# Kernel tuning notes

Hardware: AMD Instinct MI355X
Metric: run time of the kernel (lower is better)

Reference implementation:

```python
import jax, jax.numpy as jnp
import numpy as np

B, S, DQ, DK, D, H, L = 32768, 8, 64, 512, 64, 4, 4
DH = D * H  # concat head dim = 256
EPS = 1e-5
SCALE = 1.0 / float(np.sqrt(D))  # torch scales by sqrt(key.size(-1)) == sqrt(n_dim)


def _ln(x, g, b):
    m = x.mean(-1, keepdims=True)
    v = ((x - m) ** 2).mean(-1, keepdims=True)
    return (x - m) / jnp.sqrt(v + EPS) * g + b


def _mha(q, k, v, Wq, bq, Wk, bk, Wv, bv, Wo, bo):
    nb = q.shape[0]
    def tr(x, W, b):
        # [nb, s, in] -> [nb, H, s, D] (head-major split matches torch .view)
        return (x @ W + b).reshape(nb, -1, H, D).transpose(0, 2, 1, 3)
    Q, K, V = tr(q, Wq, bq), tr(k, Wk, bk), tr(v, Wv, bv)
    prob = jax.nn.softmax(jnp.einsum('bhqd,bhkd->bhqk', Q, K) * SCALE, axis=-1)
    out = jnp.einsum('bhqk,bhkd->bhqd', prob, V).transpose(0, 2, 1, 3).reshape(nb, -1, DH)
    return out @ Wo + bo, prob


def setup_inputs() -> dict:
    ki = iter(jax.random.split(jax.random.key(0), 64))
    def w(shape, fan_in):
        return jax.random.normal(next(ki), shape, jnp.float32) / np.float32(np.sqrt(fan_in))
    return {
        'query': jax.random.normal(next(ki), (B, 1, DQ), jnp.float32),
        'latent': jax.random.normal(next(ki), (B, S, DK), jnp.float32),
        'W1': w((DK, D), DK), 'b1': jnp.zeros((D,), jnp.float32),
        'Wq': w((L, D, DH), D), 'bq': jnp.zeros((L, DH), jnp.float32),
        'Wk': w((L, D, DH), D), 'bk': jnp.zeros((L, DH), jnp.float32),
        'Wv': w((L, D, DH), D), 'bv': jnp.zeros((L, DH), jnp.float32),
        'Wo': w((L, DH, D), DH), 'bo': jnp.zeros((L, D), jnp.float32),
        'fW1': w((L, D, D), D), 'fb1': jnp.zeros((L, D), jnp.float32),
        'fW2': w((L, D, D), D), 'fb2': jnp.zeros((L, D), jnp.float32),
        'g1': jnp.ones((L, D), jnp.float32), 'be1': jnp.zeros((L, D), jnp.float32),
        'g2': jnp.ones((L, D), jnp.float32), 'be2': jnp.zeros((L, D), jnp.float32),
        'cWq': w((DQ, DH), DQ), 'cbq': jnp.zeros((DH,), jnp.float32),
        'cWk': w((D, DH), D), 'cbk': jnp.zeros((DH,), jnp.float32),
        'cWv': w((D, DH), D), 'cbv': jnp.zeros((DH,), jnp.float32),
        'cWo': w((DH, D), DH), 'cbo': jnp.zeros((D,), jnp.float32),
        'Wc': w((D, 3), D), 'bc': jnp.zeros((3,), jnp.float32),
        'Ws': w((D, 1), D), 'bs': jnp.zeros((1,), jnp.float32),
    }


def reference(query, latent, W1, b1, Wq, bq, Wk, bk, Wv, bv, Wo, bo,
              fW1, fb1, fW2, fb2, g1, be1, g2, be2,
              cWq, cbq, cWk, cbk, cWv, cbv, cWo, cbo, Wc, bc, Ws, bs):
    out = jax.nn.relu(latent @ W1 + b1)  # [B, S, D]
    probs = []
    for i in range(L):
        a, p = _mha(out, out, out, Wq[i], bq[i], Wk[i], bk[i], Wv[i], bv[i], Wo[i], bo[i])
        out = _ln(a + out, g1[i], be1[i])
        ff = jax.nn.relu(out @ fW1[i] + fb1[i]) @ fW2[i] + fb2[i]  # dropout is eval-mode identity
        out = _ln(ff + out, g2[i], be2[i])
        probs.append(p)
    attn = jnp.stack(probs, axis=1)  # [B, L, H, S, S]
    sigma = jnp.max(out, axis=1) @ Ws + bs  # [B, 1]
    ca, _ = _mha(query, out, out, cWq, cbq, cWk, cbk, cWv, cbv, cWo, cbo)
    color = jax.nn.relu(ca) @ Wc + bc  # [B, 1, 3]
    return color, sigma, out, attn
```

## Files before the change

### kernel.cpp

```cpp
#include <hip/hip_runtime.h>

typedef unsigned short u16;
#define DEV __device__ __forceinline__

constexpr int B_  = 32768;
constexpr int S_  = 8;
constexpr int DK_ = 512;
constexpr int D_  = 64;
constexpr int H_  = 4;
constexpr int DH_ = 256;
constexpr int L_  = 4;
constexpr float SCALE_ = 0.125f;
constexpr float EPS_   = 1e-5f;

DEV float wsum(float x){
    #pragma unroll
    for (int m=1; m<64; m<<=1) x += __shfl_xor(x, m, 64);
    return x;
}

struct P {
    const float *query,*latent,*W1,*b1,*Wq,*bq,*Wk,*bk,*Wv,*bv,*Wo,*bo,
                *fW1,*fb1,*fW2,*fb2,*g1,*be1,*g2,*be2,
                *cWq,*cbq,*cWk,*cbk,*cWv,*cbv,*cWo,*cbo,*Wc,*bc,*Ws,*bs;
    float *o_color,*o_sigma,*o_out,*o_attn;
};

constexpr int WLDS = 512 + 2080 + 2080 + 256;

__global__ __launch_bounds__(128) void rt_fused(P p){
    __shared__ float sh[2*WLDS];
    const int wave = threadIdx.x >> 6;
    const int lane = threadIdx.x & 63;
    const int b    = blockIdx.x*2 + wave;
    float* so   = sh + wave*WLDS;
    float* bufA = so   + 512;
    float* bufK = bufA + 2080;
    float* bufP = bufK + 2080;

    float o[8];
    {
        float* lat = so;
        const float4* latv = (const float4*)(p.latent + (size_t)b*(S_*DK_));
        float4* lat4 = (float4*)lat;
        #pragma unroll
        for (int k=0;k<16;++k) lat4[k*64+lane] = latv[k*64+lane];
        __syncthreads();
        float acc[8];
        #pragma unroll
        for (int s=0;s<8;++s) acc[s] = p.b1[lane];
        #pragma unroll 4
        for (int c=0;c<512;++c){
            float w = p.W1[c*64 + lane];
            #pragma unroll
            for (int s=0;s<8;++s) acc[s] = fmaf(lat[s*512+c], w, acc[s]);
        }
        #pragma unroll
        for (int s=0;s<8;++s) o[s] = fmaxf(acc[s], 0.f);
        __syncthreads();
    }

    float v[4][8];
    for (int i=0;i<L_;++i){
        const float* Wq_i = p.Wq + (size_t)i*D_*DH_;
        const float* Wk_i = p.Wk + (size_t)i*D_*DH_;
        const float* Wv_i = p.Wv + (size_t)i*D_*DH_;
        const float* bq_i = p.bq + i*DH_;
        const float* bk_i = p.bk + i*DH_;
        const float* bv_i = p.bv + i*DH_;
        const float* Wo_i = p.Wo + (size_t)i*DH_*D_;
        const float* bo_i = p.bo + i*D_;
        const float* fW1_i= p.fW1+ i*D_*D_;
        const float* fb1_i= p.fb1+ i*D_;
        const float* fW2_i= p.fW2+ i*D_*D_;
        const float* fb2_i= p.fb2+ i*D_;
        const float* g1_i = p.g1 + i*D_;
        const float* be1_i= p.be1+ i*D_;
        const float* g2_i = p.g2 + i*D_;
        const float* be2_i= p.be2+ i*D_;

        #pragma unroll
        for (int s=0;s<8;++s) so[s*64+lane] = o[s];
        __syncthreads();

        for (int h=0;h<4;++h){
            float aq[8], ak[8], av[8];
            float bqv = bq_i[h*64+lane], bkv = bk_i[h*64+lane], bvv = bv_i[h*64+lane];
            #pragma unroll
            for (int s=0;s<8;++s){ aq[s]=bqv; ak[s]=bkv; av[s]=bvv; }
            #pragma unroll 4
            for (int c=0;c<64;++c){
                int wi = c*256 + h*64 + lane;
                float wq=Wq_i[wi], wk=Wk_i[wi], wv=Wv_i[wi];
                #pragma unroll
                for (int s=0;s<8;++s){
                    float ov = so[s*64+c];
                    aq[s]=fmaf(ov,wq,aq[s]); ak[s]=fmaf(ov,wk,ak[s]); av[s]=fmaf(ov,wv,av[s]);
                }
            }
            #pragma unroll
            for (int s=0;s<8;++s){
                bufA[(h*8+s)*65+lane]=aq[s];
                bufK[(h*8+s)*65+lane]=ak[s];
                v[h][s]=av[s];
            }
        }
        __syncthreads();

        {
            const int q = lane>>3, kk = lane&7;
            #pragma unroll
            for (int h=0;h<4;++h){
                float sc=0.f;
                #pragma unroll 8
                for (int d=0;d<64;++d) sc = fmaf(bufA[(h*8+q)*65+d], bufK[(h*8+kk)*65+d], sc);
                sc *= SCALE_;
                float mx = sc;
                mx=fmaxf(mx,__shfl_xor(mx,1,64));
                mx=fmaxf(mx,__shfl_xor(mx,2,64));
                mx=fmaxf(mx,__shfl_xor(mx,4,64));
                float e=__expf(sc-mx);
                float sm=e;
                sm+=__shfl_xor(sm,1,64); sm+=__shfl_xor(sm,2,64); sm+=__shfl_xor(sm,4,64);
                float pr=e/sm;
                p.o_attn[(size_t)b*1024 + i*256 + h*64 + lane] = pr;
                bufP[h*64+lane]=pr;
            }
        }
        __syncthreads();

        #pragma unroll
        for (int h=0;h<4;++h){
            #pragma unroll
            for (int s=0;s<8;++s){
                float acc=0.f;
                #pragma unroll
                for (int k2=0;k2<8;++k2) acc = fmaf(bufP[h*64+s*8+k2], v[h][k2], acc);
                bufA[s*256 + h*64 + lane] = acc;
            }
        }
        __syncthreads();

        {
            float acc[8];
            float bv2 = bo_i[lane];
            #pragma unroll
            for (int s=0;s<8;++s) acc[s]=bv2;
            #pragma unroll 4
            for (int p2=0;p2<256;++p2){
                float w = Wo_i[p2*64 + lane];
                #pragma unroll
                for (int s=0;s<8;++s) acc[s]=fmaf(bufA[s*256+p2], w, acc[s]);
            }
            float g=g1_i[lane], be=be1_i[lane];
            #pragma unroll
            for (int s=0;s<8;++s){
                float x = acc[s] + o[s];
                float m = wsum(x)*(1.f/64.f);
                float xm = x-m;
                float var = wsum(xm*xm)*(1.f/64.f);
                o[s] = xm*rsqrtf(var+EPS_)*g + be;
            }
        }
        __syncthreads();

        #pragma unroll
        for (int s=0;s<8;++s) so[s*64+lane]=o[s];
        __syncthreads();
        {
            float acc[8];
            float bv2=fb1_i[lane];
            #pragma unroll
            for (int s=0;s<8;++s) acc[s]=bv2;
            #pragma unroll 4
            for (int c=0;c<64;++c){
                float w=fW1_i[c*64+lane];
                #pragma unroll
                for (int s=0;s<8;++s) acc[s]=fmaf(so[s*64+c], w, acc[s]);
            }
            #pragma unroll
            for (int s=0;s<8;++s) bufK[s*64+lane]=fmaxf(acc[s],0.f);
        }
        __syncthreads();
        {
            float acc[8];
            float bv2=fb2_i[lane];
            #pragma unroll
            for (int s=0;s<8;++s) acc[s]=bv2;
            #pragma unroll 4
            for (int c=0;c<64;++c){
                float w=fW2_i[c*64+lane];
                #pragma unroll
                for (int s=0;s<8;++s) acc[s]=fmaf(bufK[s*64+c], w, acc[s]);
            }
            float g=g2_i[lane], be=be2_i[lane];
            #pragma unroll
            for (int s=0;s<8;++s){
                float x = acc[s]+o[s];
                float m=wsum(x)*(1.f/64.f);
                float xm=x-m;
                float var=wsum(xm*xm)*(1.f/64.f);
                o[s]=xm*rsqrtf(var+EPS_)*g+be;
            }
        }
        __syncthreads();
    }

    #pragma unroll
    for (int s=0;s<8;++s) p.o_out[(size_t)b*512 + s*64 + lane] = o[s];

    {
        float mx=o[0];
        #pragma unroll
        for (int s=1;s<8;++s) mx=fmaxf(mx,o[s]);
        float part = mx*p.Ws[lane];
        float sg = wsum(part) + p.bs[0];
        if (lane==0) p.o_sigma[b]=sg;
    }

    #pragma unroll
    for (int s=0;s<8;++s) so[s*64+lane]=o[s];
    bufP[lane]=p.query[(size_t)b*64 + lane];
    __syncthreads();

    float vc[4][8];
    for (int h=0;h<4;++h){
        {
            float aq=p.cbq[h*64+lane];
            #pragma unroll 4
            for (int c=0;c<64;++c) aq=fmaf(bufP[c], p.cWq[c*256 + h*64+lane], aq);
            bufA[h*65+lane]=aq;
        }
        float ak[8], av[8];
        float bkv=p.cbk[h*64+lane], bvv=p.cbv[h*64+lane];
        #pragma unroll
        for (int s=0;s<8;++s){ ak[s]=bkv; av[s]=bvv; }
        #pragma unroll 4
        for (int c=0;c<64;++c){
            int wi=c*256+h*64+lane;
            float wk=p.cWk[wi], wv=p.cWv[wi];
            #pragma unroll
            for (int s=0;s<8;++s){
                float ov=so[s*64+c];
                ak[s]=fmaf(ov,wk,ak[s]); av[s]=fmaf(ov,wv,av[s]);
            }
        }
        #pragma unroll
        for (int s=0;s<8;++s){ bufK[(h*8+s)*65+lane]=ak[s]; vc[h][s]=av[s]; }
    }
    __syncthreads();

    {
        const int hh=(lane>>3)&3, k2=lane&7;
        float sc=0.f;
        #pragma unroll 8
        for (int d=0;d<64;++d) sc=fmaf(bufA[hh*65+d], bufK[(hh*8+k2)*65+d], sc);
        sc*=SCALE_;
        float mx=sc;
        mx=fmaxf(mx,__shfl_xor(mx,1,64));
        mx=fmaxf(mx,__shfl_xor(mx,2,64));
        mx=fmaxf(mx,__shfl_xor(mx,4,64));
        float e=__expf(sc-mx);
        float sm=e;
        sm+=__shfl_xor(sm,1,64); sm+=__shfl_xor(sm,2,64); sm+=__shfl_xor(sm,4,64);
        float pr=e/sm;
        if (lane<32) bufP[lane]=pr;
    }
    __syncthreads();

    #pragma unroll
    for (int h=0;h<4;++h){
        float acc=0.f;
        #pragma unroll
        for (int k2=0;k2<8;++k2) acc=fmaf(bufP[h*8+k2], vc[h][k2], acc);
        bufA[h*64+lane]=acc;
    }
    __syncthreads();

    {
        float acc=p.cbo[lane];
        #pragma unroll 4
        for (int p2=0;p2<256;++p2) acc=fmaf(bufA[p2], p.cWo[p2*64+lane], acc);
        float r=fmaxf(acc,0.f);
        float c0=wsum(r*p.Wc[lane*3+0]);
        float c1=wsum(r*p.Wc[lane*3+1]);
        float c2=wsum(r*p.Wc[lane*3+2]);
        if (lane==0){
            p.o_color[(size_t)b*3+0]=c0+p.bc[0];
            p.o_color[(size_t)b*3+1]=c1+p.bc[1];
            p.o_color[(size_t)b*3+2]=c2+p.bc[2];
        }
    }
}

extern "C" void kernel_launch(void* const* d_in, const int* in_sizes, int n_in,
                              void* d_out, int out_size, void* d_ws, size_t ws_size,
                              hipStream_t stream){
    const float* const* ins = (const float* const*)d_in;
    P p;
    p.query=ins[0];  p.latent=ins[1]; p.W1=ins[2];   p.b1=ins[3];
    p.Wq=ins[4];     p.bq=ins[5];     p.Wk=ins[6];   p.bk=ins[7];
    p.Wv=ins[8];     p.bv=ins[9];     p.Wo=ins[10];  p.bo=ins[11];
    p.fW1=ins[12];   p.fb1=ins[13];   p.fW2=ins[14]; p.fb2=ins[15];
    p.g1=ins[16];    p.be1=ins[17];   p.g2=ins[18];  p.be2=ins[19];
    p.cWq=ins[20];   p.cbq=ins[21];   p.cWk=ins[22]; p.cbk=ins[23];
    p.cWv=ins[24];   p.cbv=ins[25];   p.cWo=ins[26]; p.cbo=ins[27];
    p.Wc=ins[28];    p.bc=ins[29];    p.Ws=ins[30];  p.bs=ins[31];
    float* out=(float*)d_out;
    p.o_color = out;
    p.o_sigma = out + (size_t)B_*3;
    p.o_out   = out + (size_t)B_*4;
    p.o_attn  = out + (size_t)B_*4 + (size_t)B_*512;
    hipLaunchKernelGGL(rt_fused, dim3(B_/2), dim3(128), 0, stream, p);
}
```

Before: 6.628 ms.

## Replace LDS staging with readlane broadcasts and fuse attention into Wo projection

Rewrites the whole fused kernel so activations stay in registers and are broadcast with readlane instead of being staged through shared memory with block barriers. The latent input is streamed in 64-column chunks with prefetch, Q/K/V are computed two heads at a time, attention output is folded straight into the Wo accumulation, and the cross-attention is recomputed per head entirely in registers. Blocks now hold 4 waves with a small per-wave LDS footprint to raise occupancy. The cost is many scalar readlane operations and higher register pressure, which could limit occupancy.

Result: faster. 6.184 ms (-6.7%).

```diff
diff --git a/kernel.cpp b/kernel.cpp
--- a/kernel.cpp
+++ b/kernel.cpp
@@ -1,17 +1,14 @@
 #include <hip/hip_runtime.h>
 
-typedef unsigned short u16;
 #define DEV __device__ __forceinline__
 
-constexpr int B_  = 32768;
-constexpr int S_  = 8;
-constexpr int DK_ = 512;
-constexpr int D_  = 64;
-constexpr int H_  = 4;
-constexpr int DH_ = 256;
-constexpr int L_  = 4;
+constexpr int B_ = 32768;
 constexpr float SCALE_ = 0.125f;
 constexpr float EPS_   = 1e-5f;
+
+DEV float rl(float x, int l){
+    return __int_as_float(__builtin_amdgcn_readlane(__float_as_int(x), l));
+}
 
 DEV float wsum(float x){
     #pragma unroll
@@ -26,269 +23,270 @@
     float *o_color,*o_sigma,*o_out,*o_attn;
 };
 
-constexpr int WLDS = 512 + 2080 + 2080 + 256;
-
-__global__ __launch_bounds__(128) void rt_fused(P p){
-    __shared__ float sh[2*WLDS];
+constexpr int WROW = 68;
+constexpr int WLDS = 2*8*WROW;
+
+__global__ __launch_bounds__(256,4) void rt_fused(P p){
+    __shared__ __align__(16) float sh[4*WLDS];
     const int wave = threadIdx.x >> 6;
     const int lane = threadIdx.x & 63;
-    const int b    = blockIdx.x*2 + wave;
-    float* so   = sh + wave*WLDS;
-    float* bufA = so   + 512;
-    float* bufK = bufA + 2080;
-    float* bufP = bufK + 2080;
+    const int b    = (blockIdx.x<<2) + wave;
+    float* lq = sh + wave*WLDS;
+    float* lk = lq + 8*WROW;
 
     float o[8];
     {
-        float* lat = so;
-        const float4* latv = (const float4*)(p.latent + (size_t)b*(S_*DK_));
-        float4* lat4 = (float4*)lat;
-        #pragma unroll
-        for (int k=0;k<16;++k) lat4[k*64+lane] = latv[k*64+lane];
-        __syncthreads();
+        const float* latb = p.latent + ((size_t)b<<12) + lane;
+        float lat[8];
+        #pragma unroll
+        for (int s=0;s<8;++s) lat[s] = latb[s*512];
         float acc[8];
-        #pragma unroll
-        for (int s=0;s<8;++s) acc[s] = p.b1[lane];
-        #pragma unroll 4
-        for (int c=0;c<512;++c){
-            float w = p.W1[c*64 + lane];
-            #pragma unroll
-            for (int s=0;s<8;++s) acc[s] = fmaf(lat[s*512+c], w, acc[s]);
+        float bb = p.b1[lane];
+        #pragma unroll
+        for (int s=0;s<8;++s) acc[s] = bb;
+        #pragma unroll 1
+        for (int cb=0; cb<8; ++cb){
+            float nlat[8];
+            if (cb < 7){
+                #pragma unroll
+                for (int s=0;s<8;++s) nlat[s] = latb[s*512 + (cb+1)*64];
+            }
+            const float* w1 = p.W1 + cb*64*64 + lane;
+            #pragma unroll 2
+            for (int c=0;c<64;++c){
+                float w = w1[c*64];
+                #pragma unroll
+                for (int s=0;s<8;++s) acc[s] = fmaf(rl(lat[s],c), w, acc[s]);
+            }
+            #pragma unroll
+            for (int s=0;s<8;++s) lat[s] = nlat[s];
         }
         #pragma unroll
         for (int s=0;s<8;++s) o[s] = fmaxf(acc[s], 0.f);
-        __syncthreads();
-    }
-
-    float v[4][8];
-    for (int i=0;i<L_;++i){
-        const float* Wq_i = p.Wq + (size_t)i*D_*DH_;
-        const float* Wk_i = p.Wk + (size_t)i*D_*DH_;
-        const float* Wv_i = p.Wv + (size_t)i*D_*DH_;
-        const float* bq_i = p.bq + i*DH_;
-        const float* bk_i = p.bk + i*DH_;
-        const float* bv_i = p.bv + i*DH_;
-        const float* Wo_i = p.Wo + (size_t)i*DH_*D_;
-        const float* bo_i = p.bo + i*D_;
-        const float* fW1_i= p.fW1+ i*D_*D_;
-        const float* fb1_i= p.fb1+ i*D_;
-        const float* fW2_i= p.fW2+ i*D_*D_;
-        const float* fb2_i= p.fb2+ i*D_;
-        const float* g1_i = p.g1 + i*D_;
-        const float* be1_i= p.be1+ i*D_;
-        const float* g2_i = p.g2 + i*D_;
-        const float* be2_i= p.be2+ i*D_;
-
-        #pragma unroll
-        for (int s=0;s<8;++s) so[s*64+lane] = o[s];
-        __syncthreads();
-
-        for (int h=0;h<4;++h){
-            float aq[8], ak[8], av[8];
-            float bqv = bq_i[h*64+lane], bkv = bk_i[h*64+lane], bvv = bv_i[h*64+lane];
-            #pragma unroll
-            for (int s=0;s<8;++s){ aq[s]=bqv; ak[s]=bkv; av[s]=bvv; }
-            #pragma unroll 4
-            for (int c=0;c<64;++c){
-                int wi = c*256 + h*64 + lane;
-                float wq=Wq_i[wi], wk=Wk_i[wi], wv=Wv_i[wi];
+    }
+
+    #pragma unroll 1
+    for (int i=0;i<4;++i){
+        const float* Wq_i = p.Wq + (size_t)i*16384;
+        const float* Wk_i = p.Wk + (size_t)i*16384;
+        const float* Wv_i = p.Wv + (size_t)i*16384;
+        const float* Wo_i = p.Wo + (size_t)i*16384;
+        const float* bq_i = p.bq + i*256;
+        const float* bk_i = p.bk + i*256;
+        const float* bv_i = p.bv + i*256;
+
+        float accO[8];
+        {
+            float bb = p.bo[i*64+lane];
+            #pragma unroll
+            for (int s=0;s<8;++s) accO[s]=bb;
+        }
+
+        #pragma unroll 1
+        for (int hg=0; hg<2; ++hg){
+            float q[2][8], k[2][8], v[2][8];
+            #pragma unroll
+            for (int u=0;u<2;++u){
+                int h = hg*2+u;
+                float bqv=bq_i[h*64+lane], bkv=bk_i[h*64+lane], bvv=bv_i[h*64+lane];
+                #pragma unroll
+                for (int s=0;s<8;++s){ q[u][s]=bqv; k[u][s]=bkv; v[u][s]=bvv; }
+            }
+            const float* wqp = Wq_i + hg*128 + lane;
+            const float* wkp = Wk_i + hg*128 + lane;
+            const float* wvp = Wv_i + hg*128 + lane;
+            #pragma unroll 2
+            for (int c=0;c<64;++c){
+                float a[8];
+                #pragma unroll
+                for (int s=0;s<8;++s) a[s]=rl(o[s],c);
+                #pragma unroll
+                for (int u=0;u<2;++u){
+                    int off = c*256 + u*64;
+                    float wq=wqp[off], wk=wkp[off], wv=wvp[off];
+                    #pragma unroll
+                    for (int s=0;s<8;++s){
+                        q[u][s]=fmaf(a[s],wq,q[u][s]);
+                        k[u][s]=fmaf(a[s],wk,k[u][s]);
+                        v[u][s]=fmaf(a[s],wv,v[u][s]);
+                    }
+                }
+            }
+            #pragma unroll
+            for (int u=0;u<2;++u){
+                const int h=hg*2+u;
                 #pragma unroll
                 for (int s=0;s<8;++s){
-                    float ov = so[s*64+c];
-                    aq[s]=fmaf(ov,wq,aq[s]); ak[s]=fmaf(ov,wk,ak[s]); av[s]=fmaf(ov,wv,av[s]);
-                }
-            }
-            #pragma unroll
-            for (int s=0;s<8;++s){
-                bufA[(h*8+s)*65+lane]=aq[s];
-                bufK[(h*8+s)*65+lane]=ak[s];
-                v[h][s]=av[s];
-            }
-        }
-        __syncthreads();
-
-        {
-            const int q = lane>>3, kk = lane&7;
-            #pragma unroll
-            for (int h=0;h<4;++h){
-                float sc=0.f;
-                #pragma unroll 8
-                for (int d=0;d<64;++d) sc = fmaf(bufA[(h*8+q)*65+d], bufK[(h*8+kk)*65+d], sc);
-                sc *= SCALE_;
-                float mx = sc;
+                    lq[s*WROW+lane]=q[u][s];
+                    lk[s*WROW+lane]=k[u][s];
+                }
+                const int qq=lane>>3, kk=lane&7;
+                float s0=0.f,s1=0.f,s2=0.f,s3=0.f;
+                #pragma unroll
+                for (int dd=0; dd<16; ++dd){
+                    float4 qa=*(const float4*)(lq + qq*WROW + dd*4);
+                    float4 kb=*(const float4*)(lk + kk*WROW + dd*4);
+                    s0=fmaf(qa.x,kb.x,s0);
+                    s1=fmaf(qa.y,kb.y,s1);
+                    s2=fmaf(qa.z,kb.z,s2);
+                    s3=fmaf(qa.w,kb.w,s3);
+                }
+                float sc=((s0+s1)+(s2+s3))*SCALE_;
+                float mx=sc;
                 mx=fmaxf(mx,__shfl_xor(mx,1,64));
                 mx=fmaxf(mx,__shfl_xor(mx,2,64));
                 mx=fmaxf(mx,__shfl_xor(mx,4,64));
                 float e=__expf(sc-mx);
                 float sm=e;
-                sm+=__shfl_xor(sm,1,64); sm+=__shfl_xor(sm,2,64); sm+=__shfl_xor(sm,4,64);
+                sm+=__shfl_xor(sm,1,64);
+                sm+=__shfl_xor(sm,2,64);
+                sm+=__shfl_xor(sm,4,64);
                 float pr=e/sm;
-                p.o_attn[(size_t)b*1024 + i*256 + h*64 + lane] = pr;
-                bufP[h*64+lane]=pr;
-            }
-        }
-        __syncthreads();
-
-        #pragma unroll
-        for (int h=0;h<4;++h){
+                p.o_attn[((size_t)b<<10) + i*256 + h*64 + lane]=pr;
+                float O[8];
+                #pragma unroll
+                for (int s=0;s<8;++s) O[s]=0.f;
+                #pragma unroll
+                for (int q2=0;q2<8;++q2){
+                    #pragma unroll
+                    for (int k2=0;k2<8;++k2)
+                        O[q2]=fmaf(rl(pr,q2*8+k2), v[u][k2], O[q2]);
+                }
+                const float* wop = Wo_i + h*64*64 + lane;
+                #pragma unroll 4
+                for (int dd=0;dd<64;++dd){
+                    float w=wop[dd*64];
+                    #pragma unroll
+                    for (int s=0;s<8;++s) accO[s]=fmaf(rl(O[s],dd), w, accO[s]);
+                }
+            }
+        }
+        {
+            float g=p.g1[i*64+lane], be=p.be1[i*64+lane];
             #pragma unroll
             for (int s=0;s<8;++s){
-                float acc=0.f;
-                #pragma unroll
-                for (int k2=0;k2<8;++k2) acc = fmaf(bufP[h*64+s*8+k2], v[h][k2], acc);
-                bufA[s*256 + h*64 + lane] = acc;
-            }
-        }
-        __syncthreads();
-
+                float x=accO[s]+o[s];
+                float m=wsum(x)*0.015625f;
+                float xm=x-m;
+                float var=wsum(xm*xm)*0.015625f;
+                o[s]=fmaf(xm*rsqrtf(var+EPS_), g, be);
+            }
+        }
         {
-            float acc[8];
-            float bv2 = bo_i[lane];
-            #pragma unroll
-            for (int s=0;s<8;++s) acc[s]=bv2;
-            #pragma unroll 4
-            for (int p2=0;p2<256;++p2){
-                float w = Wo_i[p2*64 + lane];
-                #pragma unroll
-                for (int s=0;s<8;++s) acc[s]=fmaf(bufA[s*256+p2], w, acc[s]);
-            }
-            float g=g1_i[lane], be=be1_i[lane];
+            float f1[8];
+            float bb=p.fb1[i*64+lane];
+            #pragma unroll
+            for (int s=0;s<8;++s) f1[s]=bb;
+            const float* w1p = p.fW1 + i*4096 + lane;
+            #pragma unroll 2
+            for (int c=0;c<64;++c){
+                float w=w1p[c*64];
+                #pragma unroll
+                for (int s=0;s<8;++s) f1[s]=fmaf(rl(o[s],c), w, f1[s]);
+            }
+            #pragma unroll
+            for (int s=0;s<8;++s) f1[s]=fmaxf(f1[s],0.f);
+            float f2[8];
+            float bb2=p.fb2[i*64+lane];
+            #pragma unroll
+            for (int s=0;s<8;++s) f2[s]=bb2;
+            const float* w2p = p.fW2 + i*4096 + lane;
+            #pragma unroll 2
+            for (int c=0;c<64;++c){
+                float w=w2p[c*64];
+                #pragma unroll
+                for (int s=0;s<8;++s) f2[s]=fmaf(rl(f1[s],c), w, f2[s]);
+            }
+            float g=p.g2[i*64+lane], be=p.be2[i*64+lane];
             #pragma unroll
             for (int s=0;s<8;++s){
-                float x = acc[s] + o[s];
-                float m = wsum(x)*(1.f/64.f);
-                float xm = x-m;
-                float var = wsum(xm*xm)*(1.f/64.f);
-                o[s] = xm*rsqrtf(var+EPS_)*g + be;
-            }
-        }
-        __syncthreads();
-
-        #pragma unroll
-        for (int s=0;s<8;++s) so[s*64+lane]=o[s];
-        __syncthreads();
-        {
-            float acc[8];
-            float bv2=fb1_i[lane];
-            #pragma unroll
-            for (int s=0;s<8;++s) acc[s]=bv2;
-            #pragma unroll 4
-            for (int c=0;c<64;++c){
-                float w=fW1_i[c*64+lane];
-                #pragma unroll
-                for (int s=0;s<8;++s) acc[s]=fmaf(so[s*64+c], w, acc[s]);
-            }
-            #pragma unroll
-            for (int s=0;s<8;++s) bufK[s*64+lane]=fmaxf(acc[s],0.f);
-        }
-        __syncthreads();
-        {
-            float acc[8];
-            float bv2=fb2_i[lane];
-            #pragma unroll
-            for (int s=0;s<8;++s) acc[s]=bv2;
-            #pragma unroll 4
-            for (int c=0;c<64;++c){
-                float w=fW2_i[c*64+lane];
-                #pragma unroll
-                for (int s=0;s<8;++s) acc[s]=fmaf(bufK[s*64+c], w, acc[s]);
-            }
-            float g=g2_i[lane], be=be2_i[lane];
-            #pragma unroll
-            for (int s=0;s<8;++s){
-                float x = acc[s]+o[s];
-                float m=wsum(x)*(1.f/64.f);
+                float x=f2[s]+o[s];
+                float m=wsum(x)*0.015625f;
                 float xm=x-m;
-                float var=wsum(xm*xm)*(1.f/64.f);
-                o[s]=xm*rsqrtf(var+EPS_)*g+be;
-            }
-        }
-        __syncthreads();
-    }
-
-    #pragma unroll
-    for (int s=0;s<8;++s) p.o_out[(size_t)b*512 + s*64 + lane] = o[s];
-
+                float var=wsum(xm*xm)*0.015625f;
+                o[s]=fmaf(xm*rsqrtf(var+EPS_), g, be);
+            }
+        }
+    }
+
+    {
+        float* op = p.o_out + ((size_t)b<<9) + lane;
+        #pragma unroll
+        for (int s=0;s<8;++s) op[s*64]=o[s];
+    }
     {
         float mx=o[0];
         #pragma unroll
         for (int s=1;s<8;++s) mx=fmaxf(mx,o[s]);
-        float part = mx*p.Ws[lane];
-        float sg = wsum(part) + p.bs[0];
-        if (lane==0) p.o_sigma[b]=sg;
-    }
-
-    #pragma unroll
-    for (int s=0;s<8;++s) so[s*64+lane]=o[s];
-    bufP[lane]=p.query[(size_t)b*64 + lane];
-    __syncthreads();
-
-    float vc[4][8];
-    for (int h=0;h<4;++h){
-        {
-            float aq=p.cbq[h*64+lane];
+        float sg=wsum(mx*p.Ws[lane]);
+        if (lane==0) p.o_sigma[b]=sg+p.bs[0];
+    }
+    {
+        float qr = p.query[((size_t)b<<6)+lane];
+        float accC = p.cbo[lane];
+        #pragma unroll 1
+        for (int h=0;h<4;++h){
+            float q0=p.cbq[h*64+lane], q1=0.f,q2=0.f,q3=0.f;
+            const float* wq = p.cWq + h*64 + lane;
             #pragma unroll 4
-            for (int c=0;c<64;++c) aq=fmaf(bufP[c], p.cWq[c*256 + h*64+lane], aq);
-            bufA[h*65+lane]=aq;
-        }
-        float ak[8], av[8];
-        float bkv=p.cbk[h*64+lane], bvv=p.cbv[h*64+lane];
-        #pragma unroll
-        for (int s=0;s<8;++s){ ak[s]=bkv; av[s]=bvv; }
-        #pragma unroll 4
-        for (int c=0;c<64;++c){
-            int wi=c*256+h*64+lane;
-            float wk=p.cWk[wi], wv=p.cWv[wi];
-            #pragma unroll
-            for (int s=0;s<8;++s){
-                float ov=so[s*64+c];
-                ak[s]=fmaf(ov,wk,ak[s]); av[s]=fmaf(ov,wv,av[s]);
-            }
-        }
-        #pragma unroll
-        for (int s=0;s<8;++s){ bufK[(h*8+s)*65+lane]=ak[s]; vc[h][s]=av[s]; }
-    }
-    __syncthreads();
-
-    {
-        const int hh=(lane>>3)&3, k2=lane&7;
-        float sc=0.f;
-        #pragma unroll 8
-        for (int d=0;d<64;++d) sc=fmaf(bufA[hh*65+d], bufK[(hh*8+k2)*65+d], sc);
-        sc*=SCALE_;
-        float mx=sc;
-        mx=fmaxf(mx,__shfl_xor(mx,1,64));
-        mx=fmaxf(mx,__shfl_xor(mx,2,64));
-        mx=fmaxf(mx,__shfl_xor(mx,4,64));
-        float e=__expf(sc-mx);
-        float sm=e;
-        sm+=__shfl_xor(sm,1,64); sm+=__shfl_xor(sm,2,64); sm+=__shfl_xor(sm,4,64);
-        float pr=e/sm;
-        if (lane<32) bufP[lane]=pr;
-    }
-    __syncthreads();
-
-    #pragma unroll
-    for (int h=0;h<4;++h){
-        float acc=0.f;
-        #pragma unroll
-        for (int k2=0;k2<8;++k2) acc=fmaf(bufP[h*8+k2], vc[h][k2], acc);
-        bufA[h*64+lane]=acc;
-    }
-    __syncthreads();
-
-    {
-        float acc=p.cbo[lane];
-        #pragma unroll 4
-        for (int p2=0;p2<256;++p2) acc=fmaf(bufA[p2], p.cWo[p2*64+lane], acc);
-        float r=fmaxf(acc,0.f);
+            for (int c=0;c<64;c+=4){
+                q0=fmaf(rl(qr,c+0), wq[(c+0)*256], q0);
+                q1=fmaf(rl(qr,c+1), wq[(c+1)*256], q1);
+                q2=fmaf(rl(qr,c+2), wq[(c+2)*256], q2);
+                q3=fmaf(rl(qr,c+3), wq[(c+3)*256], q3);
+            }
+            float Qc=(q0+q1)+(q2+q3);
+            float Kc[8], Vc[8];
+            float bkv=p.cbk[h*64+lane], bvv=p.cbv[h*64+lane];
+            #pragma unroll
+            for (int s=0;s<8;++s){ Kc[s]=bkv; Vc[s]=bvv; }
+            const float* wk = p.cWk + h*64 + lane;
+            const float* wv = p.cWv + h*64 + lane;
+            #pragma unroll 2
+            for (int c=0;c<64;++c){
+                float a[8];
+                #pragma unroll
+                for (int s=0;s<8;++s) a[s]=rl(o[s],c);
+                float wkv=wk[c*256], wvv=wv[c*256];
+                #pragma unroll
+                for (int s=0;s<8;++s){
+                    Kc[s]=fmaf(a[s],wkv,Kc[s]);
+                    Vc[s]=fmaf(a[s],wvv,Vc[s]);
+                }
+            }
+            float scs[8];
+            #pragma unroll
+            for (int s=0;s<8;++s) scs[s]=wsum(Qc*Kc[s])*SCALE_;
+            float m=scs[0];
+            #pragma unroll
+            for (int s=1;s<8;++s) m=fmaxf(m,scs[s]);
+            float e[8], sm=0.f;
+            #pragma unroll
+            for (int s=0;s<8;++s){ e[s]=__expf(scs[s]-m); sm+=e[s]; }
+            float inv=1.f/sm;
+            float Oc=0.f;
+            #pragma unroll
+            for (int s=0;s<8;++s) Oc=fmaf(e[s]*inv, Vc[s], Oc);
+            const float* wo = p.cWo + h*64*64 + lane;
+            float a0=0.f,a1=0.f,a2=0.f,a3=0.f;
+            #pragma unroll 4
+            for (int dd=0;dd<64;dd+=4){
+                a0=fmaf(rl(Oc,dd+0), wo[(dd+0)*64], a0);
+                a1=fmaf(rl(Oc,dd+1), wo[(dd+1)*64], a1);
+                a2=fmaf(rl(Oc,dd+2), wo[(dd+2)*64], a2);
+                a3=fmaf(rl(Oc,dd+3), wo[(dd+3)*64], a3);
+            }
+            accC += (a0+a1)+(a2+a3);
+        }
+        float r=fmaxf(accC,0.f);
         float c0=wsum(r*p.Wc[lane*3+0]);
         float c1=wsum(r*p.Wc[lane*3+1]);
         float c2=wsum(r*p.Wc[lane*3+2]);
         if (lane==0){
-            p.o_color[(size_t)b*3+0]=c0+p.bc[0];
-            p.o_color[(size_t)b*3+1]=c1+p.bc[1];
-            p.o_color[(size_t)b*3+2]=c2+p.bc[2];
+            float* oc = p.o_color + (size_t)b*3;
+            oc[0]=c0+p.bc[0];
+            oc[1]=c1+p.bc[1];
+            oc[2]=c2+p.bc[2];
         }
     }
 }
@@ -311,5 +309,5 @@
     p.o_sigma = out + (size_t)B_*3;
     p.o_out   = out + (size_t)B_*4;
     p.o_attn  = out + (size_t)B_*4 + (size_t)B_*512;
-    hipLaunchKernelGGL(rt_fused, dim3(B_/2), dim3(128), 0, stream, p);
+    hipLaunchKernelGGL(rt_fused, dim3(B_/4), dim3(256), 0, stream, p);
 }
```
